# Kernel optimization log

Hardware: AMD Instinct MI355X
Metric: run time of the kernel (lower is better)

## Reference

```python
import jax, jax.numpy as jnp
import numpy as np
import math

NUM_HEADS = 16
NUM_KV_HEADS = 4
HEAD_DIM = 128
HIDDEN = 2048
ROPE_BASE = 10000.0


def setup_inputs() -> dict:
    key = jax.random.key(0)
    ks = jax.random.split(key, 6)
    B, S = 1, 4096
    hidden_states = jax.random.normal(ks[0], (B, S, HIDDEN), dtype=jnp.float32)
    attention_mask = jnp.ones((B, S), dtype=jnp.int32)
    position_ids = jnp.broadcast_to(jnp.arange(S, dtype=jnp.int32)[None, :], (B, S))
    sc = 1.0 / math.sqrt(HIDDEN)
    wq = jax.random.normal(ks[1], (HIDDEN, NUM_HEADS * HEAD_DIM), dtype=jnp.float32) * sc
    wk = jax.random.normal(ks[2], (HIDDEN, NUM_KV_HEADS * HEAD_DIM), dtype=jnp.float32) * sc
    wv = jax.random.normal(ks[3], (HIDDEN, NUM_KV_HEADS * HEAD_DIM), dtype=jnp.float32) * sc
    wo = jax.random.normal(ks[4], (NUM_HEADS * HEAD_DIM, HIDDEN), dtype=jnp.float32) * sc
    return {"hidden_states": hidden_states, "attention_mask": attention_mask,
            "position_ids": position_ids, "wq": wq, "wk": wk, "wv": wv, "wo": wo}


def _rotate_half(x):
    x1, x2 = jnp.split(x, 2, axis=-1)
    return jnp.concatenate((-x2, x1), axis=-1)


def _rope_tables(seq_len, dtype):
    inv_freq = 1.0 / (ROPE_BASE ** (jnp.arange(0, HEAD_DIM, 2, dtype=jnp.float32) / HEAD_DIM))
    t = jnp.arange(seq_len, dtype=jnp.float32)
    freqs = jnp.outer(t, inv_freq)                       # [S, hd/2]
    emb = jnp.concatenate((freqs, freqs), axis=-1)       # [S, hd]
    return jnp.cos(emb).astype(dtype), jnp.sin(emb).astype(dtype)


def reference(hidden_states, attention_mask, position_ids, wq, wk, wv, wo):
    B, S, _ = hidden_states.shape
    dtype = hidden_states.dtype
    # projections -> [B, H, S, hd]
    q = (hidden_states @ wq).reshape(B, S, NUM_HEADS, HEAD_DIM).transpose(0, 2, 1, 3)
    k = (hidden_states @ wk).reshape(B, S, NUM_KV_HEADS, HEAD_DIM).transpose(0, 2, 1, 3)
    v = (hidden_states @ wv).reshape(B, S, NUM_KV_HEADS, HEAD_DIM).transpose(0, 2, 1, 3)
    # RoPE
    cos_t, sin_t = _rope_tables(S, dtype)
    cos = cos_t[position_ids][:, None]                   # [B,1,S,hd]
    sin = sin_t[position_ids][:, None]
    q = q * cos + _rotate_half(q) * sin
    k = k * cos + _rotate_half(k) * sin
    # GQA repeat
    n_rep = NUM_HEADS // NUM_KV_HEADS
    k = jnp.repeat(k, n_rep, axis=1)
    v = jnp.repeat(v, n_rep, axis=1)
    # scores + causal mask + padding mask
    scores = jnp.einsum('bhqd,bhkd->bhqk', q, k) / math.sqrt(HEAD_DIM)
    neg = jnp.finfo(scores.dtype).min
    causal = jnp.triu(jnp.full((S, S), neg, dtype=scores.dtype), k=1)
    scores = scores + causal[None, None]
    pad = (1.0 - attention_mask.astype(scores.dtype))[:, None, None, :] * neg
    scores = scores + pad
    attn = jax.nn.softmax(scores.astype(jnp.float32), axis=-1).astype(dtype)
    out = jnp.einsum('bhqk,bhkd->bhqd', attn, v)
    out = out.transpose(0, 2, 1, 3).reshape(B, S, NUM_HEADS * HEAD_DIM)
    return out @ wo
```

## Files before the change

kernel.cpp:

```cpp
#include <hip/hip_runtime.h>
#include <cstdint>
#include <cstddef>

typedef unsigned short ushort_t;
typedef short    bf16x8 __attribute__((ext_vector_type(8)));
typedef float    f32x4  __attribute__((ext_vector_type(4)));
typedef uint4    __attribute__((may_alias)) uint4_a;
typedef ushort4  __attribute__((may_alias)) ushort4_a;
typedef float4   __attribute__((may_alias)) float4_a;
typedef float2   __attribute__((may_alias)) float2_a;
typedef unsigned __attribute__((may_alias)) uint_a;

constexpr int SEQ = 4096, HID = 2048, NHEADS = 16, NKVH = 4, HDIM = 128;
constexpr int QD  = NHEADS * HDIM;
constexpr int KVD = NKVH * HDIM;
constexpr int KVL = 2 * KVD;
constexpr int NPART = 56;

static __device__ __forceinline__ float bf2f(ushort_t u) {
    return __uint_as_float(((unsigned)u) << 16);
}
static __device__ __forceinline__ ushort_t f2bf(float f) {
    unsigned x = __float_as_uint(f);
    unsigned r = x + 0x7FFFu + ((x >> 16) & 1u);
    return (ushort_t)(r >> 16);
}
static __device__ __forceinline__ unsigned pack2(float lo, float hi) {
    return (unsigned)f2bf(lo) | ((unsigned)f2bf(hi) << 16);
}
static __device__ __forceinline__ unsigned cvt_pk(float lo, float hi) {
    unsigned r;
    asm("v_cvt_pk_bf16_f32 %0, %1, %2" : "=v"(r) : "v"(lo), "v"(hi));
    return r;
}

static __device__ __forceinline__ void gld16(const ushort_t* g, ushort_t* l) {
    __builtin_amdgcn_global_load_lds(
        (const __attribute__((address_space(1))) unsigned*)g,
        (__attribute__((address_space(3))) unsigned*)l, 16, 0, 0);
}

__global__ __launch_bounds__(256) void cast_f32_bf16(
    const float* __restrict__ in, ushort_t* __restrict__ out, int n)
{
    int i = (blockIdx.x * 256 + threadIdx.x) * 8;
    if (i >= n) return;
    float4 a = *(const float4_a*)(in + i);
    float4 b = *(const float4_a*)(in + i + 4);
    uint4 o;
    o.x = pack2(a.x, a.y); o.y = pack2(a.z, a.w);
    o.z = pack2(b.x, b.y); o.w = pack2(b.z, b.w);
    *(uint4_a*)(out + i) = o;
}

__global__ __launch_bounds__(256) void transpose_cast(
    const float* __restrict__ W, ushort_t* __restrict__ WT, int K, int N)
{
    __shared__ float tl[32][36];
    const int k0 = blockIdx.x * 32, n0 = blockIdx.y * 32;
    const int t  = threadIdx.x;
    {
        int i = t >> 3, jb = (t & 7) * 4;
        *(float4_a*)&tl[i][jb] = *(const float4_a*)(W + (size_t)(k0 + i) * N + n0 + jb);
    }
    __syncthreads();
    {
        int n = t >> 3, kb = (t & 7) * 4;
        ushort4 o;
        o.x = f2bf(tl[kb + 0][n]); o.y = f2bf(tl[kb + 1][n]);
        o.z = f2bf(tl[kb + 2][n]); o.w = f2bf(tl[kb + 3][n]);
        *(ushort4_a*)(WT + (size_t)(n0 + n) * K + k0 + kb) = o;
    }
}

__global__ __launch_bounds__(256) void gemm_mfma(
    const ushort_t* __restrict__ A, int lda,
    const ushort_t* __restrict__ Bt, int ldb,
    void* __restrict__ C1, int ld1, void* __restrict__ C2, int ld2,
    int split, int N, int K, int out_f32)
{
    __shared__ ushort_t as[128 * 32];
    __shared__ ushort_t bs[128 * 32];

    const int t    = threadIdx.x;
    const int mb   = blockIdx.y * 128, nb = blockIdx.x * 128;
    const int w    = t >> 6, lane = t & 63, quad = lane >> 4, l15 = lane & 15;
    const int wm   = (w >> 1) * 64, wn = (w & 1) * 64;

    const int dr_row = lane >> 2, dr_c = lane & 3;
    const int rA0 = w * 16 + dr_row, rA1 = 64 + w * 16 + dr_row;
    const ushort_t* a0p = A  + (size_t)(mb + rA0) * lda + (dr_c ^ (rA0 & 3)) * 8;
    const ushort_t* a1p = A  + (size_t)(mb + rA1) * lda + (dr_c ^ (rA1 & 3)) * 8;
    const ushort_t* b0p = Bt + (size_t)(nb + rA0) * ldb + (dr_c ^ (rA0 & 3)) * 8;
    const ushort_t* b1p = Bt + (size_t)(nb + rA1) * ldb + (dr_c ^ (rA1 & 3)) * 8;
    ushort_t* asb0 = &as[(w) * 512];        ushort_t* asb1 = &as[(4 + w) * 512];
    ushort_t* bsb0 = &bs[(w) * 512];        ushort_t* bsb1 = &bs[(4 + w) * 512];

    f32x4 acc[4][4];
#pragma unroll
    for (int i = 0; i < 4; i++)
#pragma unroll
        for (int j = 0; j < 4; j++) acc[i][j] = (f32x4)0.f;

    const int chunk = quad ^ (l15 & 3);

    for (int kb = 0; kb < K; kb += 32) {
        __syncthreads();
        gld16(a0p + kb, asb0);
        gld16(a1p + kb, asb1);
        gld16(b0p + kb, bsb0);
        gld16(b1p + kb, bsb1);
        __syncthreads();

        bf16x8 af[4], bf[4];
#pragma unroll
        for (int mt = 0; mt < 4; mt++)
            af[mt] = *(const bf16x8*)&as[(wm + mt * 16 + l15) * 32 + chunk * 8];
#pragma unroll
        for (int nt = 0; nt < 4; nt++)
            bf[nt] = *(const bf16x8*)&bs[(wn + nt * 16 + l15) * 32 + chunk * 8];
#pragma unroll
        for (int mt = 0; mt < 4; mt++)
#pragma unroll
            for (int nt = 0; nt < 4; nt++)
                acc[mt][nt] = __builtin_amdgcn_mfma_f32_16x16x32_bf16(
                    af[mt], bf[nt], acc[mt][nt], 0, 0, 0);
    }

#pragma unroll
    for (int mt = 0; mt < 4; mt++)
#pragma unroll
        for (int nt = 0; nt < 4; nt++) {
            int colg = nb + wn + nt * 16 + l15;
#pragma unroll
            for (int r = 0; r < 4; r++) {
                int row = mb + wm + mt * 16 + quad * 4 + r;
                float v = acc[mt][nt][r];
                if (out_f32)            ((float*)C1)[(size_t)row * ld1 + colg] = v;
                else if (colg < split)  ((ushort_t*)C1)[(size_t)row * ld1 + colg] = f2bf(v);
                else                    ((ushort_t*)C2)[(size_t)row * ld2 + colg - split] = f2bf(v);
            }
        }
}

__global__ __launch_bounds__(256) void rope_bf16(
    ushort_t* __restrict__ buf, int ld, int nh, const int* __restrict__ pos_ids)
{
    int idx  = blockIdx.x * 256 + threadIdx.x;
    int i    = idx & 63;
    int rem  = idx >> 6;
    int head = rem % nh;
    int s    = rem / nh;
    if (s >= SEQ) return;

    float pos = (float)pos_ids[s];
    float ang = pos * __expf(-(float)i * 0.14391156831212787f);
    float c, sn;
    sincosf(ang, &sn, &c);

    ushort_t* p = buf + (size_t)s * ld + head * HDIM;
    float x0 = bf2f(p[i]);
    float x1 = bf2f(p[i + 64]);
    p[i]      = f2bf(x0 * c - x1 * sn);
    p[i + 64] = f2bf(x1 * c + x0 * sn);
}

__global__ __launch_bounds__(512, 4) void flash_mfma(
    const ushort_t* Q, const ushort_t* __restrict__ KV,
    const int* __restrict__ amask, ushort_t* O,
    ushort_t* __restrict__ Opart, float2* __restrict__ ML)
{
    __shared__ ushort_t ks[64][136];
    __shared__ ushort_t vt[128][72];
    __shared__ float    bias[64];

    const int t = threadIdx.x, w = t >> 6, lane = t & 63;
    const int quad = lane >> 4, l15 = lane & 15;
    const int h = blockIdx.x, kvh = h >> 2;
    const int s = blockIdx.y;
    const int kcol = kvh * HDIM, vcol = KVD + kvh * HDIM;
    const float scale2 = 0.08838834764831845f * 1.44269504088896340f;

    int tile, ktb, kte, pid;
    bool multi;
    if (s < 8)       { tile = 15 - s;        ktb = 0; kte = 2 * tile + 2; multi = false; pid = 0; }
    else if (s < 64) {
        int cs = s - 8;
        int c;
        if (cs < 24) { tile = 16 + cs / 3; c = cs - (tile - 16) * 3; }
        else         { int d = cs - 24; tile = 24 + (d >> 2); c = d & 3; }
        int nkt = 2 * tile + 2;
        ktb = c * 16; kte = (ktb + 16 < nkt) ? ktb + 16 : nkt;
        multi = true; pid = h * NPART + cs;
    }
    else             { tile = 7 - (s - 64);  ktb = 0; kte = 2 * tile + 2; multi = false; pid = 0; }

    const int q0  = tile * 128;
    const int q0w = q0 + w * 16;

    const int krow = t >> 3,  kdo = (t & 7) * 16;
    const int vkp  = t & 31,  vdg = t >> 5;

    int bpi[4];
#pragma unroll
    for (int t4 = 0; t4 < 4; t4++)
        bpi[t4] = ((2 * (quad & 1) + (t4 >> 1)) * 16 + l15) * 4;
    const bool hi_half = (quad >> 1) != 0;

    bf16x8 qf[4];
    {
        const ushort_t* qp = Q + (size_t)(q0w + l15) * QD + h * HDIM;
#pragma unroll
        for (int c = 0; c < 4; c++)
            qf[c] = *(const bf16x8*)(qp + c * 32 + quad * 8);
    }

    f32x4 accO[8];
#pragma unroll
    for (int j = 0; j < 8; j++) accO[j] = (f32x4)0.f;
    float m_s = -1e30f, l_s = 0.f;

    uint4 kst[2], va, vb;
    float bst = 0.f;
    auto stage_load = [&](int kt) {
        const int k0 = kt * 64;
        const ushort_t* kp = KV + (size_t)(k0 + krow) * KVL + kcol + kdo;
        kst[0] = *(const uint4_a*)kp;
        kst[1] = *(const uint4_a*)(kp + 8);
        const ushort_t* vp = KV + (size_t)(k0 + 2 * vkp) * KVL + vcol + vdg * 8;
        va = *(const uint4_a*)vp;
        vb = *(const uint4_a*)(vp + KVL);
        if (t < 64) bst = amask[k0 + t] ? 0.f : -1e30f;
    };

    stage_load(ktb);

    for (int kt = ktb; kt < kte; kt++) {
        const int k0 = kt * 64;
        __syncthreads();
        *(uint4_a*)&ks[krow][kdo]     = kst[0];
        *(uint4_a*)&ks[krow][kdo + 8] = kst[1];
        {
            unsigned aw[4] = {va.x, va.y, va.z, va.w};
            unsigned bw[4] = {vb.x, vb.y, vb.z, vb.w};
#pragma unroll
            for (int i = 0; i < 4; i++) {
                *(uint_a*)&vt[vdg * 8 + 2 * i][2 * vkp] =
                    (aw[i] & 0xFFFFu) | (bw[i] << 16);
                *(uint_a*)&vt[vdg * 8 + 2 * i + 1][2 * vkp] =
                    (aw[i] >> 16) | (bw[i] & 0xFFFF0000u);
            }
        }
        if (t < 64) bias[t] = bst;
        __syncthreads();
        if (kt + 1 < kte) stage_load(kt + 1);

        if (k0 > q0w + 15) continue;

        f32x4 sx[4];
#pragma unroll
        for (int mt = 0; mt < 4; mt++) sx[mt] = (f32x4)0.f;
#pragma unroll
        for (int c = 0; c < 4; c++)
#pragma unroll
            for (int mt = 0; mt < 4; mt++) {
                bf16x8 kf = *(const bf16x8*)&ks[mt * 16 + l15][c * 32 + quad * 8];
                sx[mt] = __builtin_amdgcn_mfma_f32_16x16x32_bf16(kf, qf[c], sx[mt], 0, 0, 0);
            }

        const int qg = q0w + l15;
        const bool full = (k0 + 63 <= q0w);
        float p[4][4];
        float mx = -1e30f;
#pragma unroll
        for (int mt = 0; mt < 4; mt++) {
            float4 b4 = *(const float4_a*)&bias[mt * 16 + quad * 4];
            float br[4] = {b4.x, b4.y, b4.z, b4.w};
#pragma unroll
            for (int r = 0; r < 4; r++) {
                float v = fmaf(sx[mt][r], scale2, br[r]);
                if (!full) {
                    int kg = k0 + mt * 16 + quad * 4 + r;
                    v = (kg > qg) ? -1e30f : v;
                }
                p[mt][r] = v;
                mx = fmaxf(mx, v);
            }
        }
        mx = fmaxf(mx, __shfl_xor(mx, 16));
        mx = fmaxf(mx, __shfl_xor(mx, 32));
        const bool renorm = !__all(mx <= m_s + 8.f);
        const float mnew = renorm ? fmaxf(m_s, mx) : m_s;
        float sum = 0.f;
        unsigned wlo[4], whi[4];
#pragma unroll
        for (int mt = 0; mt < 4; mt++) {
            float p0 = exp2f(p[mt][0] - mnew);
            float p1 = exp2f(p[mt][1] - mnew);
            float p2 = exp2f(p[mt][2] - mnew);
            float p3 = exp2f(p[mt][3] - mnew);
            sum += (p0 + p1) + (p2 + p3);
            wlo[mt] = cvt_pk(p0, p1);
            whi[mt] = cvt_pk(p2, p3);
        }
        sum += __shfl_xor(sum, 16);
        sum += __shfl_xor(sum, 32);

        if (renorm) {
            float alpha = exp2f(m_s - mnew);
            l_s *= alpha;
            float a0 = __shfl(alpha, quad * 4 + 0);
            float a1 = __shfl(alpha, quad * 4 + 1);
            float a2 = __shfl(alpha, quad * 4 + 2);
            float a3 = __shfl(alpha, quad * 4 + 3);
#pragma unroll
            for (int j = 0; j < 8; j++) {
                f32x4 a = accO[j];
                a[0] *= a0; a[1] *= a1; a[2] *= a2; a[3] *= a3;
                accO[j] = a;
            }
        }
        m_s = mnew;
        l_s += sum;

#pragma unroll
        for (int kc = 0; kc < 2; kc++) {
            union { unsigned u[4]; bf16x8 v; } pf;
#pragma unroll
            for (int t4 = 0; t4 < 4; t4++) {
                unsigned slo = (t4 & 1) ? whi[2 * kc]     : wlo[2 * kc];
                unsigned shi = (t4 & 1) ? whi[2 * kc + 1] : wlo[2 * kc + 1];
                int ra = __builtin_amdgcn_ds_bpermute(bpi[t4], (int)slo);
                int rb = __builtin_amdgcn_ds_bpermute(bpi[t4], (int)shi);
                pf.u[t4] = (unsigned)(hi_half ? rb : ra);
            }
#pragma unroll
            for (int n8 = 0; n8 < 8; n8++) {
                bf16x8 vf = *(const bf16x8*)&vt[n8 * 16 + l15][kc * 32 + quad * 8];
                accO[n8] = __builtin_amdgcn_mfma_f32_16x16x32_bf16(pf.v, vf, accO[n8], 0, 0, 0);
            }
        }
    }

    if (!multi) {
        float linv = 1.0f / l_s;
#pragma unroll
        for (int r = 0; r < 4; r++) {
            float lr = __shfl(linv, quad * 4 + r);
            int row = q0w + quad * 4 + r;
            ushort_t* op = O + (size_t)row * QD + h * HDIM;
#pragma unroll
            for (int n8 = 0; n8 < 8; n8++)
                op[n8 * 16 + l15] = f2bf(accO[n8][r] * lr);
        }
    } else {
        ushort_t* op = Opart + (size_t)pid * (128 * 128);
#pragma unroll
        for (int r = 0; r < 4; r++) {
            int row = w * 16 + quad * 4 + r;
#pragma unroll
            for (int n8 = 0; n8 < 8; n8++)
                op[row * 128 + n8 * 16 + l15] = f2bf(accO[n8][r]);
        }
        if (quad == 0)
            ML[pid * 128 + w * 16 + l15] = make_float2(m_s, l_s);
    }
}

__global__ __launch_bounds__(256) void combine_partials(
    const ushort_t* __restrict__ P, const float2* __restrict__ ML,
    ushort_t* __restrict__ O)
{
    const int h = blockIdx.x >> 4, tt = blockIdx.x & 15, tile = 16 + tt;
    const int nc = (tile < 24) ? 3 : 4;
    const int pid0 = h * NPART + ((tile < 24) ? tt * 3 : 24 + (tile - 24) * 4);
    const int tid = threadIdx.x;
    const int row = tid >> 1, dh = (tid & 1) << 6;

    float m_[4], l_[4];
    float M = -1e30f;
#pragma unroll
    for (int c = 0; c < 4; c++) {
        if (c < nc) {
            float2 v = *(const float2_a*)&ML[(pid0 + c) * 128 + row];
            m_[c] = v.x; l_[c] = v.y; M = fmaxf(M, v.x);
        } else { m_[c] = -1e30f; l_[c] = 0.f; }
    }
    float L = 0.f, wgt[4];
#pragma unroll
    for (int c = 0; c < 4; c++) { wgt[c] = exp2f(m_[c] - M); L += wgt[c] * l_[c]; }
    const float inv = 1.0f / L;

    ushort_t* op = O + (size_t)(tile * 128 + row) * QD + h * HDIM + dh;
    const size_t pbase = (size_t)row * 128 + dh;
#pragma unroll
    for (int g = 0; g < 8; g++) {
        float acc[8] = {0.f, 0.f, 0.f, 0.f, 0.f, 0.f, 0.f, 0.f};
#pragma unroll
        for (int c = 0; c < 4; c++) {
            if (c < nc) {
                const ushort_t* pp = P + (size_t)(pid0 + c) * (128 * 128) + pbase + g * 8;
                uint4 v = *(const uint4_a*)pp;
                unsigned u[4] = {v.x, v.y, v.z, v.w};
#pragma unroll
                for (int j = 0; j < 4; j++) {
                    acc[2 * j]     += wgt[c] * bf2f((ushort_t)(u[j] & 0xFFFFu));
                    acc[2 * j + 1] += wgt[c] * bf2f((ushort_t)(u[j] >> 16));
                }
            }
        }
        uint4 o;
        o.x = pack2(acc[0] * inv, acc[1] * inv); o.y = pack2(acc[2] * inv, acc[3] * inv);
        o.z = pack2(acc[4] * inv, acc[5] * inv); o.w = pack2(acc[6] * inv, acc[7] * inv);
        *(uint4_a*)(op + g * 8) = o;
    }
}

extern "C" void kernel_launch(void* const* d_in, const int* in_sizes, int n_in,
                              void* d_out, int out_size, void* d_ws, size_t ws_size,
                              hipStream_t stream)
{
    const float* x     = (const float*)d_in[0];
    const int*   amask = (const int*)d_in[1];
    const int*   pos   = (const int*)d_in[2];
    const float* wq    = (const float*)d_in[3];
    const float* wk    = (const float*)d_in[4];
    const float* wv    = (const float*)d_in[5];
    const float* wo    = (const float*)d_in[6];
    float* out = (float*)d_out;

    ushort_t* wqkvT = (ushort_t*)d_out;
    ushort_t* xb    = wqkvT + (size_t)3072 * HID;

    ushort_t* qbuf  = (ushort_t*)d_ws;
    ushort_t* kvbuf = qbuf + (size_t)SEQ * QD;
    ushort_t* woT   = kvbuf;

    ushort_t* opart = (ushort_t*)d_out;
    float2*   mlbuf = (float2*)((char*)d_out + (size_t)16 * NPART * 128 * 128 * 2);

    cast_f32_bf16<<<SEQ * HID / 8 / 256, 256, 0, stream>>>(x, xb, SEQ * HID);
    transpose_cast<<<dim3(HID / 32, QD / 32),  256, 0, stream>>>(wq, wqkvT, HID, QD);
    transpose_cast<<<dim3(HID / 32, KVD / 32), 256, 0, stream>>>(wk, wqkvT + (size_t)QD * HID, HID, KVD);
    transpose_cast<<<dim3(HID / 32, KVD / 32), 256, 0, stream>>>(wv, wqkvT + (size_t)(QD + KVD) * HID, HID, KVD);

    gemm_mfma<<<dim3(3072 / 128, SEQ / 128), 256, 0, stream>>>(
        xb, HID, wqkvT, HID, qbuf, QD, kvbuf, KVL, QD, 3072, HID, 0);

    rope_bf16<<<SEQ * NHEADS * 64 / 256, 256, 0, stream>>>(qbuf, QD, NHEADS, pos);
    rope_bf16<<<SEQ * NKVH  * 64 / 256, 256, 0, stream>>>(kvbuf, KVL, NKVH, pos);

    flash_mfma<<<dim3(NHEADS, 72), 512, 0, stream>>>(
        qbuf, kvbuf, amask, qbuf, opart, mlbuf);
    combine_partials<<<dim3(256), 256, 0, stream>>>(opart, mlbuf, qbuf);

    transpose_cast<<<dim3(QD / 32, HID / 32), 256, 0, stream>>>(wo, woT, QD, HID);
    gemm_mfma<<<dim3(HID / 128, SEQ / 128), 256, 0, stream>>>(
        qbuf, QD, woT, QD, out, HID, out, HID, HID, HID, QD, 1);
}
```

Measured before the change: 467.4 us.

## Fuse RoPE launches, raise wave priority around MFMA, restructure partial combine

Merges the two RoPE kernels into a single launch covering both Q and K heads, removing one launch and its tail. Wraps the QK^T and PV MFMA loops in the flash kernel with s_setprio(1)/s_setprio(0) so waves issuing matrix ops get scheduling priority over waves doing softmax and loads. Rewrites combine_partials to compute the per-row combine weights once into shared memory, then have all threads do coalesced 16-element loads and stores with the weights already normalized. Costs are an extra barrier and a branch on head index in RoPE, and the priority hints may have no effect depending on how waves interleave.

```diff
diff --git a/kernel.cpp b/kernel.cpp
--- a/kernel.cpp
+++ b/kernel.cpp
@@ -143,14 +143,15 @@
         }
 }
 
-__global__ __launch_bounds__(256) void rope_bf16(
-    ushort_t* __restrict__ buf, int ld, int nh, const int* __restrict__ pos_ids)
+__global__ __launch_bounds__(256) void rope_both(
+    ushort_t* __restrict__ qb, ushort_t* __restrict__ kvb,
+    const int* __restrict__ pos_ids)
 {
     int idx  = blockIdx.x * 256 + threadIdx.x;
     int i    = idx & 63;
     int rem  = idx >> 6;
-    int head = rem % nh;
-    int s    = rem / nh;
+    int hs   = rem % (NHEADS + NKVH);
+    int s    = rem / (NHEADS + NKVH);
     if (s >= SEQ) return;
 
     float pos = (float)pos_ids[s];
@@ -158,7 +159,9 @@
     float c, sn;
     sincosf(ang, &sn, &c);
 
-    ushort_t* p = buf + (size_t)s * ld + head * HDIM;
+    ushort_t* p = (hs < NHEADS)
+        ? qb  + (size_t)s * QD  + hs * HDIM
+        : kvb + (size_t)s * KVL + (hs - NHEADS) * HDIM;
     float x0 = bf2f(p[i]);
     float x1 = bf2f(p[i + 64]);
     p[i]      = f2bf(x0 * c - x1 * sn);
@@ -260,6 +263,7 @@
         f32x4 sx[4];
 #pragma unroll
         for (int mt = 0; mt < 4; mt++) sx[mt] = (f32x4)0.f;
+        __builtin_amdgcn_s_setprio(1);
 #pragma unroll
         for (int c = 0; c < 4; c++)
 #pragma unroll
@@ -267,6 +271,7 @@
                 bf16x8 kf = *(const bf16x8*)&ks[mt * 16 + l15][c * 32 + quad * 8];
                 sx[mt] = __builtin_amdgcn_mfma_f32_16x16x32_bf16(kf, qf[c], sx[mt], 0, 0, 0);
             }
+        __builtin_amdgcn_s_setprio(0);
 
         const int qg = q0w + l15;
         const bool full = (k0 + 63 <= q0w);
@@ -334,11 +339,13 @@
                 int rb = __builtin_amdgcn_ds_bpermute(bpi[t4], (int)shi);
                 pf.u[t4] = (unsigned)(hi_half ? rb : ra);
             }
+            __builtin_amdgcn_s_setprio(1);
 #pragma unroll
             for (int n8 = 0; n8 < 8; n8++) {
                 bf16x8 vf = *(const bf16x8*)&vt[n8 * 16 + l15][kc * 32 + quad * 8];
                 accO[n8] = __builtin_amdgcn_mfma_f32_16x16x32_bf16(pf.v, vf, accO[n8], 0, 0, 0);
             }
+            __builtin_amdgcn_s_setprio(0);
         }
     }
 
@@ -371,48 +378,63 @@
     const ushort_t* __restrict__ P, const float2* __restrict__ ML,
     ushort_t* __restrict__ O)
 {
+    __shared__ float wc[4][128];
     const int h = blockIdx.x >> 4, tt = blockIdx.x & 15, tile = 16 + tt;
     const int nc = (tile < 24) ? 3 : 4;
     const int pid0 = h * NPART + ((tile < 24) ? tt * 3 : 24 + (tile - 24) * 4);
     const int tid = threadIdx.x;
-    const int row = tid >> 1, dh = (tid & 1) << 6;
-
-    float m_[4], l_[4];
-    float M = -1e30f;
-#pragma unroll
-    for (int c = 0; c < 4; c++) {
-        if (c < nc) {
-            float2 v = *(const float2_a*)&ML[(pid0 + c) * 128 + row];
-            m_[c] = v.x; l_[c] = v.y; M = fmaxf(M, v.x);
-        } else { m_[c] = -1e30f; l_[c] = 0.f; }
-    }
-    float L = 0.f, wgt[4];
-#pragma unroll
-    for (int c = 0; c < 4; c++) { wgt[c] = exp2f(m_[c] - M); L += wgt[c] * l_[c]; }
-    const float inv = 1.0f / L;
-
-    ushort_t* op = O + (size_t)(tile * 128 + row) * QD + h * HDIM + dh;
-    const size_t pbase = (size_t)row * 128 + dh;
-#pragma unroll
-    for (int g = 0; g < 8; g++) {
-        float acc[8] = {0.f, 0.f, 0.f, 0.f, 0.f, 0.f, 0.f, 0.f};
+
+    if (tid < 128) {
+        const int row = tid;
+        float m_[4], l_[4];
+        float M = -1e30f;
 #pragma unroll
         for (int c = 0; c < 4; c++) {
             if (c < nc) {
-                const ushort_t* pp = P + (size_t)(pid0 + c) * (128 * 128) + pbase + g * 8;
-                uint4 v = *(const uint4_a*)pp;
-                unsigned u[4] = {v.x, v.y, v.z, v.w};
-#pragma unroll
-                for (int j = 0; j < 4; j++) {
-                    acc[2 * j]     += wgt[c] * bf2f((ushort_t)(u[j] & 0xFFFFu));
-                    acc[2 * j + 1] += wgt[c] * bf2f((ushort_t)(u[j] >> 16));
+                float2 v = *(const float2_a*)&ML[(pid0 + c) * 128 + row];
+                m_[c] = v.x; l_[c] = v.y; M = fmaxf(M, v.x);
+            } else { m_[c] = -1e30f; l_[c] = 0.f; }
+        }
+        float L = 0.f, wgt[4];
+#pragma unroll
+        for (int c = 0; c < 4; c++) { wgt[c] = exp2f(m_[c] - M); L += wgt[c] * l_[c]; }
+        const float inv = 1.0f / L;
+#pragma unroll
+        for (int c = 0; c < 4; c++) wc[c][row] = (c < nc) ? wgt[c] * inv : 0.f;
+    }
+    __syncthreads();
+
+#pragma unroll
+    for (int p = 0; p < 4; p++) {
+        const int idx = p * 256 + tid;
+        const int row = idx >> 3, seg = idx & 7;
+        const size_t pb = (size_t)row * 128 + seg * 16;
+        float acc[16];
+#pragma unroll
+        for (int j = 0; j < 16; j++) acc[j] = 0.f;
+#pragma unroll
+        for (int c = 0; c < 4; c++) {
+            if (c < nc) {
+                const ushort_t* pp = P + (size_t)(pid0 + c) * (128 * 128) + pb;
+                uint4 v0 = *(const uint4_a*)pp;
+                uint4 v1 = *(const uint4_a*)(pp + 8);
+                const float wv_ = wc[c][row];
+                unsigned u[8] = {v0.x, v0.y, v0.z, v0.w, v1.x, v1.y, v1.z, v1.w};
+#pragma unroll
+                for (int j = 0; j < 8; j++) {
+                    acc[2 * j]     += wv_ * bf2f((ushort_t)(u[j] & 0xFFFFu));
+                    acc[2 * j + 1] += wv_ * bf2f((ushort_t)(u[j] >> 16));
                 }
             }
         }
-        uint4 o;
-        o.x = pack2(acc[0] * inv, acc[1] * inv); o.y = pack2(acc[2] * inv, acc[3] * inv);
-        o.z = pack2(acc[4] * inv, acc[5] * inv); o.w = pack2(acc[6] * inv, acc[7] * inv);
-        *(uint4_a*)(op + g * 8) = o;
+        ushort_t* op = O + (size_t)(tile * 128 + row) * QD + h * HDIM + seg * 16;
+        uint4 o0, o1;
+        o0.x = pack2(acc[0],  acc[1]);  o0.y = pack2(acc[2],  acc[3]);
+        o0.z = pack2(acc[4],  acc[5]);  o0.w = pack2(acc[6],  acc[7]);
+        o1.x = pack2(acc[8],  acc[9]);  o1.y = pack2(acc[10], acc[11]);
+        o1.z = pack2(acc[12], acc[13]); o1.w = pack2(acc[14], acc[15]);
+        *(uint4_a*)op       = o0;
+        *(uint4_a*)(op + 8) = o1;
     }
 }
 
@@ -447,8 +469,7 @@
     gemm_mfma<<<dim3(3072 / 128, SEQ / 128), 256, 0, stream>>>(
         xb, HID, wqkvT, HID, qbuf, QD, kvbuf, KVL, QD, 3072, HID, 0);
 
-    rope_bf16<<<SEQ * NHEADS * 64 / 256, 256, 0, stream>>>(qbuf, QD, NHEADS, pos);
-    rope_bf16<<<SEQ * NKVH  * 64 / 256, 256, 0, stream>>>(kvbuf, KVL, NKVH, pos);
+    rope_both<<<SEQ * (NHEADS + NKVH) * 64 / 256, 256, 0, stream>>>(qbuf, kvbuf, pos);
 
     flash_mfma<<<dim3(NHEADS, 72), 512, 0, stream>>>(
         qbuf, kvbuf, amask, qbuf, opart, mlbuf);
```

Measured after the change: 449.2 us. 3.9% less time.
